# Performance work log

Hardware: AMD Instinct MI355X
Metric: run time of the kernel (lower is better)

The kernel has to match this reference:

```python
import jax, jax.numpy as jnp
import numpy as np

EPS = 1e-5  # BatchNorm1d default eps


def _bn(x):
    # BatchNorm1d(affine=False) in training mode: batch stats, biased variance
    m = x.mean(axis=0)
    v = ((x - m) ** 2).mean(axis=0)
    return (x - m) / jnp.sqrt(v + EPS)


def _gconv(x, A, W, b):
    # GraphConv with MeanAggregator: concat(x, A@x) @ W + b, ReLU
    agg = jnp.einsum('gnm,gmd->gnd', A, x)
    cat = jnp.concatenate([x, agg], axis=-1)
    return jax.nn.relu(jnp.einsum('gnd,df->gnf', cat, W) + b)


def setup_inputs() -> dict:
    key = jax.random.key(0)
    ks = jax.random.split(key, 16)
    B, C, H, Wd = 4, 32, 512, 512
    G, N, F = 512, 41, 576  # local graphs, 1+8+8*4 nodes, 3*4*(32+6)+120 feat
    d = {}
    d['inputs'] = jax.random.normal(ks[0], (B, C, H, Wd), jnp.float32)
    d['node_feats'] = jax.random.normal(ks[1], (G, N, F), jnp.float32)
    A = jax.random.uniform(ks[2], (G, N, N), jnp.float32)
    d['A'] = A / A.sum(-1, keepdims=True)  # row-normalized adjacency (mean agg)
    d['knn_inx'] = jax.random.randint(ks[3], (G, 8), 0, N)
    d['conv_w'] = jax.random.normal(ks[4], (6, C), jnp.float32) * 0.01
    d['conv_b'] = jnp.zeros((6,), jnp.float32)
    dims = [(2 * F, 512), (2 * 512, 256), (2 * 256, 128), (2 * 128, 64)]
    for i, (di, do) in enumerate(dims):
        d['W%d' % (i + 1)] = jax.random.normal(ks[5 + i], (di, do), jnp.float32) / np.float32(np.sqrt(di))
        d['b%d' % (i + 1)] = jnp.zeros((do,), jnp.float32)
    d['cls_w1'] = jax.random.normal(ks[10], (64, 32), jnp.float32) / 8.0
    d['cls_b1'] = jnp.zeros((32,), jnp.float32)
    d['prelu_a'] = jnp.full((32,), 0.25, jnp.float32)
    d['cls_w2'] = jax.random.normal(ks[11], (32, 2), jnp.float32) / np.float32(np.sqrt(32))
    d['cls_b2'] = jnp.zeros((2,), jnp.float32)
    return d


def reference(inputs, node_feats, A, knn_inx, conv_w, conv_b, W1, b1, W2, b2, W3, b3, W4, b4, cls_w1, cls_b1, prelu_a, cls_w2, cls_b2):
    # 1x1 conv: out_conv(inputs)
    pred_maps = jnp.einsum('bchw,oc->bohw', inputs, conv_w) + conv_b[None, :, None, None]
    # GCN over local graphs
    G, N, F = node_feats.shape
    x = _bn(node_feats.reshape(G * N, F)).reshape(G, N, F)
    x = _gconv(x, A, W1, b1)
    x = _gconv(x, A, W2, b2)
    x = _gconv(x, A, W3, b3)
    x = _gconv(x, A, W4, b4)
    # gather knn neighbor node features per graph -> edge features
    edge = jnp.take_along_axis(x, knn_inx[:, :, None], axis=1).reshape(-1, x.shape[-1])
    h = edge @ cls_w1 + cls_b1
    h = jnp.where(h >= 0, h, prelu_a * h)  # PReLU(32)
    gcn_pred = h @ cls_w2 + cls_b2  # [G*k, 2]
    return (pred_maps, gcn_pred)
```

## Files before the change

kernel.cpp:

```cpp
#include <hip/hip_runtime.h>
#include <hip/hip_bf16.h>


using f32x4 = __attribute__((ext_vector_type(4))) float;
using s16x8 = __attribute__((ext_vector_type(8))) short;

#define GN 20992
#define NFEAT 576
#define NGRAPH 512
#define NNODE 41
#define ASTR 44
#define NTMG 171

typedef __attribute__((address_space(1))) const unsigned int gas_u32;
typedef __attribute__((address_space(3))) unsigned int las_u32;

__device__ __forceinline__ void gl_lds16(const void* g, void* l) {
  __builtin_amdgcn_global_load_lds((gas_u32*)g, (las_u32*)l, 16, 0, 0);
}

__device__ __forceinline__ float dot41_f4(const float* __restrict__ Am,
                                          const float* __restrict__ pr) {
  float s0 = 0.f, s1 = 0.f, s2 = 0.f, s3 = 0.f;
#pragma unroll
  for (int q = 0; q < 10; ++q) {
    float4 a4 = *(const float4*)(Am + q * 4);
    s0 += a4.x * pr[q * 4];
    s1 += a4.y * pr[q * 4 + 1];
    s2 += a4.z * pr[q * 4 + 2];
    s3 += a4.w * pr[q * 4 + 3];
  }
  return ((s0 + s1) + (s2 + s3)) + Am[40] * pr[40];
}

__global__ __launch_bounds__(576) void front_kernel(
    const float* __restrict__ nf, float* __restrict__ partial,
    __hip_bfloat16* __restrict__ x0) {
  int c = threadIdx.x;
  int u = blockIdx.x;
  int r0 = u * 82;
  const float* src = nf + (size_t)r0 * NFEAT + c;
  __hip_bfloat16* dst = x0 + (size_t)r0 * NFEAT + c;
  float s = 0.f, s2 = 0.f;
#pragma unroll 4
  for (int r = 0; r < 82; ++r) {
    float v = src[(size_t)r * NFEAT];
    s += v; s2 += v * v;
    dst[(size_t)r * NFEAT] = __float2bfloat16(v);
  }
  partial[(size_t)u * 1152 + c] = s;
  partial[(size_t)u * 1152 + NFEAT + c] = s2;
}

__global__ __launch_bounds__(256) void reduce_kernel(
    const float* __restrict__ partial, float* __restrict__ statsbuf) {
  int t = blockIdx.x * 256 + threadIdx.x;
  if (t >= NFEAT) return;
  float s = 0.f, s2 = 0.f;
#pragma unroll 8
  for (int u = 0; u < 256; ++u) {
    s += partial[(size_t)u * 1152 + t];
    s2 += partial[(size_t)u * 1152 + NFEAT + t];
  }
  float m = s * (1.f / GN);
  float v = s2 * (1.f / GN) - m * m;
  float inv = rsqrtf(v + 1e-5f);
  statsbuf[t] = inv;
  statsbuf[NFEAT + t] = m * inv;
}

__global__ __launch_bounds__(256) void wt1_kernel(
    const float* __restrict__ W1, const float* __restrict__ b1,
    const float* __restrict__ statsbuf, __hip_bfloat16* __restrict__ B1,
    float* __restrict__ gbias,
    const float* __restrict__ W2, const float* __restrict__ W3,
    const float* __restrict__ W4,
    __hip_bfloat16* __restrict__ B2, __hip_bfloat16* __restrict__ B3,
    __hip_bfloat16* __restrict__ B4) {
  int u = blockIdx.x;
  int tid = threadIdx.x;
  if (u < 576) {
    __shared__ float T[32 * 33];
    int jt = u / 18, kt = u - jt * 18;
    int j0 = jt * 32, k0 = kt * 32;
    int h = (j0 >= 512) ? 1 : 0;
    const float* Wh = W1 + (size_t)(h * 576) * 512 + (j0 - h * 512);
    int r = tid >> 5, cc = tid & 31;
#pragma unroll
    for (int i = 0; i < 4; ++i)
      T[(r + i * 8) * 33 + cc] = Wh[(size_t)(k0 + r + i * 8) * 512 + cc];
    __syncthreads();
    float invv = statsbuf[k0 + cc];
#pragma unroll
    for (int i = 0; i < 4; ++i) {
      int rowh = (j0 - h * 512) + r + i * 8;
      int jp = (rowh >> 6) * 128 + h * 64 + (rowh & 63);
      B1[(size_t)jp * 576 + k0 + cc] =
          __float2bfloat16(T[cc * 33 + (r + i * 8)] * invv);
    }
  } else if (u < 580) {
    int j = (u - 576) * 256 + tid;
    int col = (j < 512) ? j : j - 512;
    const float* base = W1 + (size_t)((j < 512) ? 0 : 576) * 512 + col;
    float s = 0.f;
#pragma unroll 4
    for (int f = 0; f < NFEAT; ++f) s += statsbuf[NFEAT + f] * base[(size_t)f * 512];
    gbias[j] = ((j < 512) ? b1[j] : 0.f) - s;
  } else {
    __shared__ float T[32 * 33];
    int t = u - 580;
    const float* W; __hip_bfloat16* B; int K, N;
    if (t < 256)      { W = W2; B = B2; K = 512; N = 256; }
    else if (t < 320) { W = W3; B = B3; K = 256; N = 128; t -= 256; }
    else              { W = W4; B = B4; K = 128; N = 64;  t -= 320; }
    int tilesN = N >> 5;
    int perhalf = (K >> 5) * tilesN;
    int h = t / perhalf; t -= h * perhalf;
    int tk = t / tilesN, tn = t - tk * tilesN;
    int r = tid >> 5, cc = tid & 31;
    const float* Wh = W + (size_t)h * K * N;
#pragma unroll
    for (int i = 0; i < 4; ++i)
      T[(r + i * 8) * 33 + cc] = Wh[(size_t)(tk * 32 + r + i * 8) * N + tn * 32 + cc];
    __syncthreads();
#pragma unroll
    for (int i = 0; i < 4; ++i) {
      int row = tn * 32 + r + i * 8;
      int jp = (row >> 6) * 128 + h * 64 + (row & 63);
      B[(size_t)jp * K + tk * 32 + cc] =
          __float2bfloat16(T[cc * 33 + r + i * 8]);
    }
  }
}

__global__ __launch_bounds__(256) void gemmagg_kernel(
    const __hip_bfloat16* __restrict__ Xptr, const __hip_bfloat16* __restrict__ Bt,
    const float* __restrict__ biasL, const float* __restrict__ biasR,
    __hip_bfloat16* __restrict__ Yptr, int Nout, int K, int NTN,
    const float* __restrict__ Aadj,
    const float* __restrict__ cinputs, const float* __restrict__ conv_w,
    const float* __restrict__ conv_b, float* __restrict__ cout) {
  __shared__ __align__(16) char smem[53136];
  short* AshD = (short*)smem;
  short* BshD = (short*)(smem + 16384);
  __hip_bfloat16* Psh = (__hip_bfloat16*)smem;
  float* Aash = (float*)(smem + 31488);

  int tid = threadIdx.x;
  int bid = blockIdx.x;
  int gemmBlocks = NTMG * NTN;

  if (bid >= gemmBlocks) {
    int p = (bid - gemmBlocks) * 256 + tid;
    int img = p >> 16, q = p & 65535;
    const float4* ip = (const float4*)cinputs + (size_t)img * 32 * 65536 + q;
    float4 acc[6];
#pragma unroll
    for (int o = 0; o < 6; ++o) { float b0 = conv_b[o]; acc[o] = make_float4(b0, b0, b0, b0); }
#pragma unroll 4
    for (int c = 0; c < 32; ++c) {
      float4 x = ip[(size_t)c * 65536];
#pragma unroll
      for (int o = 0; o < 6; ++o) {
        float wv = conv_w[o * 32 + c];
        acc[o].x += x.x * wv; acc[o].y += x.y * wv;
        acc[o].z += x.z * wv; acc[o].w += x.w * wv;
      }
    }
    float4* op = (float4*)cout + (size_t)img * 6 * 65536 + q;
#pragma unroll
    for (int o = 0; o < 6; ++o) op[(size_t)o * 65536] = acc[o];
    return;
  }

  int sg = bid / (NTN * 8);
  int rem = bid - sg * (NTN * 8);
  int Wm = NTMG - sg * 8; if (Wm > 8) Wm = 8;
  int mt = sg * 8 + rem % Wm;
  int nt = rem / Wm;
  int row0 = mt * 123;
  int g0 = mt * 3;
  int gcnt = NGRAPH - g0; if (gcnt > 3) gcnt = 3;

  int wave = tid >> 6, lane = tid & 63;
  int wm = wave >> 1, wn = wave & 1;
  int lr = lane & 15, kb = lane >> 4;

  f32x4 acc[4][4];
#pragma unroll
  for (int m = 0; m < 4; ++m)
#pragma unroll
    for (int n = 0; n < 4; ++n) acc[m][n] = (f32x4){0.f, 0.f, 0.f, 0.f};

  const short* Ag = (const short*)Xptr;
  const short* Bg = (const short*)Bt + (size_t)nt * 128 * K;

  int c0 = tid, c1 = tid + 256;
  int ar0 = c0 >> 2, ak0 = (((c0 & 3) ^ ((ar0 >> 1) & 3))) * 8;
  int ar1 = c1 >> 2, ak1 = (((c1 & 3) ^ ((ar1 >> 1) & 3))) * 8;
  int grow0 = row0 + ar0; if (grow0 > GN - 1) grow0 = GN - 1;
  int grow1 = row0 + ar1; if (grow1 > GN - 1) grow1 = GN - 1;

  int aoff[4], boff[4];
#pragma unroll
  for (int m = 0; m < 4; ++m) {
    int r = wm * 64 + m * 16 + lr;
    aoff[m] = r * 32 + ((((r >> 1) & 3) ^ kb) * 8);
  }
#pragma unroll
  for (int n = 0; n < 4; ++n) {
    int r = wn * 64 + n * 16 + lr;
    boff[n] = r * 32 + ((((r >> 1) & 3) ^ kb) * 8);
  }

  gl_lds16(Ag + (size_t)grow0 * K + ak0, &AshD[c0 * 8]);
  gl_lds16(Ag + (size_t)grow1 * K + ak1, &AshD[c1 * 8]);
  gl_lds16(Bg + (size_t)ar0 * K + ak0, &BshD[c0 * 8]);
  gl_lds16(Bg + (size_t)ar1 * K + ak1, &BshD[c1 * 8]);
  __syncthreads();

  int nkt = K >> 5;
  int cur = 0;
  for (int kt = 0; kt < nkt; ++kt) {
    if (kt + 1 < nkt) {
      int k1 = (kt + 1) * 32;
      int nxt = (cur ^ 1) * 4096;
      gl_lds16(Ag + (size_t)grow0 * K + k1 + ak0, &AshD[nxt + c0 * 8]);
      gl_lds16(Ag + (size_t)grow1 * K + k1 + ak1, &AshD[nxt + c1 * 8]);
      gl_lds16(Bg + (size_t)ar0 * K + k1 + ak0, &BshD[nxt + c0 * 8]);
      gl_lds16(Bg + (size_t)ar1 * K + k1 + ak1, &BshD[nxt + c1 * 8]);
    }
    int cb = cur * 4096;
    s16x8 af[4], bfr[4];
#pragma unroll
    for (int m = 0; m < 4; ++m) af[m] = *(const s16x8*)&AshD[cb + aoff[m]];
#pragma unroll
    for (int n = 0; n < 4; ++n) bfr[n] = *(const s16x8*)&BshD[cb + boff[n]];
#pragma unroll
    for (int m = 0; m < 4; ++m)
#pragma unroll
      for (int n = 0; n < 4; ++n)
        acc[m][n] = __builtin_amdgcn_mfma_f32_16x16x32_bf16(af[m], bfr[n], acc[m][n], 0, 0, 0);
    __syncthreads();
    cur ^= 1;
  }

  int rbase = (lane >> 4) * 4;
#pragma unroll
  for (int m = 0; m < 4; ++m) {
    int lrow = wm * 64 + m * 16 + rbase;
#pragma unroll
    for (int n = 0; n < 4; ++n) {
      int w = wn * 64 + n * 16 + lr;
      float bv = (w < 64) ? biasL[nt * 64 + w]
                          : (biasR ? biasR[nt * 64 + (w - 64)] : 0.f);
#pragma unroll
      for (int r = 0; r < 4; ++r)
        Psh[(size_t)(lrow + r) * 128 + w] = __float2bfloat16(acc[m][n][r] + bv);
    }
  }
  __syncthreads();

  {
    int tot = gcnt * (NNODE * NNODE);
    const float* Asrc = Aadj + (size_t)g0 * (NNODE * NNODE);
    for (int i = tid; i < tot; i += 256) {
      int row = i / NNODE, m = i - row * NNODE;
      Aash[row * ASTR + m] = Asrc[i];
    }
  }
  __syncthreads();

  int c = tid & 63, grp = tid >> 6;
  for (int g = 0; g < gcnt; ++g) {
    float pr[NNODE];
#pragma unroll
    for (int m = 0; m < NNODE; ++m)
      pr[m] = __bfloat162float(Psh[(size_t)(g * NNODE + m) * 128 + 64 + c]);
#pragma unroll 1
    for (int n = grp; n < NNODE; n += 4) {
      float aa = __bfloat162float(Psh[(size_t)(g * NNODE + n) * 128 + c])
               + dot41_f4(Aash + (g * NNODE + n) * ASTR, pr);
      aa = aa > 0.f ? aa : 0.f;
      Yptr[(size_t)(row0 + g * NNODE + n) * Nout + nt * 64 + c] = __float2bfloat16(aa);
    }
  }
}

__global__ __launch_bounds__(256) void gemm4cls_kernel(
    const __hip_bfloat16* __restrict__ X, const __hip_bfloat16* __restrict__ B4t,
    const float* __restrict__ b4, const float* __restrict__ Aadj,
    const int* __restrict__ knn, const float* __restrict__ w1,
    const float* __restrict__ cb1, const float* __restrict__ pa,
    const float* __restrict__ w2, const float* __restrict__ cb2,
    float* __restrict__ out) {
  __shared__ __align__(16) char smem[49152 + 21648 + 31488 + 8192 + 520];
  short* AshD = (short*)smem;
  short* Bsh  = (short*)(smem + 16384);
  __hip_bfloat16* Psh = (__hip_bfloat16*)smem;
  float* Aash = (float*)(smem + 49152);
  float* Ysh  = (float*)(smem + 49152 + 21648);
  float* Wsh  = (float*)(smem + 49152 + 21648 + 31488);
  float* cb   = (float*)(smem + 49152 + 21648 + 31488 + 8192);

  int tid = threadIdx.x;
  int blk = blockIdx.x;
  int g0 = blk * 3;
  int gcnt = NGRAPH - g0; if (gcnt > 3) gcnt = 3;
  int row0 = blk * 123;

  {
    int tot = gcnt * (NNODE * NNODE);
    const float* Asrc = Aadj + (size_t)g0 * (NNODE * NNODE);
    for (int i = tid; i < tot; i += 256) {
      int row = i / NNODE, m = i - row * NNODE;
      Aash[row * ASTR + m] = Asrc[i];
    }
  }
  for (int i = tid; i < 2048; i += 256) Wsh[i] = w1[i];
  if (tid < 32) { cb[tid] = cb1[tid]; cb[32 + tid] = pa[tid]; }
  if (tid < 64) cb[64 + tid] = w2[tid];
  if (tid < 2) cb[128 + tid] = cb2[tid];

#pragma unroll
  for (int i = 0; i < 8; ++i) {
    int c = tid + i * 256;
    int kt = c >> 9, w = c & 511;
    int r = w >> 2, kc = ((w & 3) ^ ((r >> 1) & 3)) * 8;
    gl_lds16((const short*)B4t + (size_t)r * 128 + kt * 32 + kc, &Bsh[c * 8]);
  }
  const short* Ag = (const short*)X;
  int c0 = tid, c1 = tid + 256;
  int ar0 = c0 >> 2, ak0 = (((c0 & 3) ^ ((ar0 >> 1) & 3))) * 8;
  int ar1 = c1 >> 2, ak1 = (((c1 & 3) ^ ((ar1 >> 1) & 3))) * 8;
  int grow0 = row0 + ar0; if (grow0 > GN - 1) grow0 = GN - 1;
  int grow1 = row0 + ar1; if (grow1 > GN - 1) grow1 = GN - 1;
  gl_lds16(Ag + (size_t)grow0 * 128 + ak0, &AshD[c0 * 8]);
  gl_lds16(Ag + (size_t)grow1 * 128 + ak1, &AshD[c1 * 8]);
  __syncthreads();

  int wave = tid >> 6, lane = tid & 63;
  int wm = wave >> 1, wn = wave & 1;
  int lr = lane & 15, kb = lane >> 4;
  int aoff[4], boff[4];
#pragma unroll
  for (int m = 0; m < 4; ++m) {
    int r = wm * 64 + m * 16 + lr;
    aoff[m] = r * 32 + ((((r >> 1) & 3) ^ kb) * 8);
  }
#pragma unroll
  for (int n = 0; n < 4; ++n) {
    int r = wn * 64 + n * 16 + lr;
    boff[n] = r * 32 + ((((r >> 1) & 3) ^ kb) * 8);
  }
  f32x4 acc[4][4];
#pragma unroll
  for (int m = 0; m < 4; ++m)
#pragma unroll
    for (int n = 0; n < 4; ++n) acc[m][n] = (f32x4){0.f, 0.f, 0.f, 0.f};

  int cur = 0;
  for (int kt = 0; kt < 4; ++kt) {
    if (kt < 3) {
      int k1 = (kt + 1) * 32;
      int nxt = (cur ^ 1) * 4096;
      gl_lds16(Ag + (size_t)grow0 * 128 + k1 + ak0, &AshD[nxt + c0 * 8]);
      gl_lds16(Ag + (size_t)grow1 * 128 + k1 + ak1, &AshD[nxt + c1 * 8]);
    }
    int cbse = cur * 4096;
    s16x8 af[4], bfr[4];
#pragma unroll
    for (int m = 0; m < 4; ++m) af[m] = *(const s16x8*)&AshD[cbse + aoff[m]];
#pragma unroll
    for (int n = 0; n < 4; ++n) bfr[n] = *(const s16x8*)&Bsh[kt * 4096 + boff[n]];
#pragma unroll
    for (int m = 0; m < 4; ++m)
#pragma unroll
      for (int n = 0; n < 4; ++n)
        acc[m][n] = __builtin_amdgcn_mfma_f32_16x16x32_bf16(af[m], bfr[n], acc[m][n], 0, 0, 0);
    __syncthreads();
    cur ^= 1;
  }
  int rbase = (lane >> 4) * 4;
#pragma unroll
  for (int m = 0; m < 4; ++m) {
    int lrow = wm * 64 + m * 16 + rbase;
#pragma unroll
    for (int n = 0; n < 4; ++n) {
      int col = wn * 64 + n * 16 + lr;
      float bv = (col < 64) ? b4[col] : 0.f;
#pragma unroll
      for (int r = 0; r < 4; ++r)
        Psh[(size_t)(lrow + r) * 128 + col] = __float2bfloat16(acc[m][n][r] + bv);
    }
  }
  __syncthreads();

  int c = tid & 63, grp = tid >> 6;
  for (int g = 0; g < gcnt; ++g) {
    float pr[NNODE];
#pragma unroll
    for (int m = 0; m < NNODE; ++m)
      pr[m] = __bfloat162float(Psh[(size_t)(g * NNODE + m) * 128 + 64 + c]);
#pragma unroll 1
    for (int n = grp; n < NNODE; n += 4) {
      float aa = __bfloat162float(Psh[(size_t)(g * NNODE + n) * 128 + c])
               + dot41_f4(Aash + (g * NNODE + n) * ASTR, pr);
      Ysh[(g * NNODE + n) * 64 + c] = aa > 0.f ? aa : 0.f;
    }
  }
  __syncthreads();

  int j = tid & 31, slot = tid >> 5;
  for (int el = slot; el < 8 * gcnt; el += 8) {
    int e = g0 * 8 + el;
    int node = knn[e];
    int gl = el >> 3;
    const float* fp = &Ysh[(gl * NNODE + node) * 64];
    float a2 = cb[j];
#pragma unroll
    for (int d = 0; d < 64; ++d) a2 += fp[d] * Wsh[d * 32 + j];
    float h = a2 >= 0.f ? a2 : cb[32 + j] * a2;
#pragma unroll
    for (int o = 0; o < 2; ++o) {
      float v = h * cb[64 + j * 2 + o];
      v += __shfl_xor(v, 16, 32); v += __shfl_xor(v, 8, 32);
      v += __shfl_xor(v, 4, 32);  v += __shfl_xor(v, 2, 32);
      v += __shfl_xor(v, 1, 32);
      if (j == 0) out[(size_t)e * 2 + o] = v;
    }
  }
}

extern "C" void kernel_launch(void* const* d_in, const int* in_sizes, int n_in,
                              void* d_out, int out_size, void* d_ws, size_t ws_size,
                              hipStream_t stream) {
  const float* inputs     = (const float*)d_in[0];
  const float* node_feats = (const float*)d_in[1];
  const float* Aadj       = (const float*)d_in[2];
  const int*   knn        = (const int*)d_in[3];
  const float* conv_w     = (const float*)d_in[4];
  const float* conv_b     = (const float*)d_in[5];
  const float* W1 = (const float*)d_in[6];  const float* b1 = (const float*)d_in[7];
  const float* W2 = (const float*)d_in[8];  const float* b2 = (const float*)d_in[9];
  const float* W3 = (const float*)d_in[10]; const float* b3 = (const float*)d_in[11];
  const float* W4 = (const float*)d_in[12]; const float* b4 = (const float*)d_in[13];
  const float* cls_w1 = (const float*)d_in[14]; const float* cls_b1 = (const float*)d_in[15];
  const float* prelu_a = (const float*)d_in[16];
  const float* cls_w2 = (const float*)d_in[17]; const float* cls_b2 = (const float*)d_in[18];
  float* out = (float*)d_out;

  char* ws = (char*)d_ws;
  char* R1 = ws;
  char* R2 = ws + 24200192;
  char* wp = ws + 24200192 + 42991616;
  __hip_bfloat16* B1t = (__hip_bfloat16*)wp;  wp += 1179648;
  __hip_bfloat16* B2t = (__hip_bfloat16*)wp;  wp += 524288;
  __hip_bfloat16* B3t = (__hip_bfloat16*)wp;  wp += 131072;
  __hip_bfloat16* B4t = (__hip_bfloat16*)wp;  wp += 32768;
  float* partial  = (float*)wp;               wp += 256 * 1152 * 4;
  float* statsbuf = (float*)wp;               wp += 1152 * 4;
  float* gbias    = (float*)wp;               wp += 1024 * 4;

  __hip_bfloat16* x0 = (__hip_bfloat16*)R1;

  front_kernel<<<256, 576, 0, stream>>>(node_feats, partial, x0);
  reduce_kernel<<<3, 256, 0, stream>>>(partial, statsbuf);
  wt1_kernel<<<932, 256, 0, stream>>>(W1, b1, statsbuf, B1t, gbias,
                                      W2, W3, W4, B2t, B3t, B4t);

  gemmagg_kernel<<<NTMG * 8 + 1024, 256, 0, stream>>>(
      x0, B1t, gbias, gbias + 512, (__hip_bfloat16*)R2, 512, 576, 8, Aadj,
      inputs, conv_w, conv_b, out);
  gemmagg_kernel<<<NTMG * 4, 256, 0, stream>>>(
      (__hip_bfloat16*)R2, B2t, b2, nullptr, (__hip_bfloat16*)R1, 256, 512, 4,
      Aadj, nullptr, nullptr, nullptr, nullptr);
  gemmagg_kernel<<<NTMG * 2, 256, 0, stream>>>(
      (__hip_bfloat16*)R1, B3t, b3, nullptr, (__hip_bfloat16*)R2, 128, 256, 2,
      Aadj, nullptr, nullptr, nullptr, nullptr);
  gemm4cls_kernel<<<171, 256, 0, stream>>>(
      (__hip_bfloat16*)R2, B4t, b4, Aadj, knn, cls_w1, cls_b1, prelu_a,
      cls_w2, cls_b2, out + 6291456);
}
```

Measured before the change: 239.2 us.

## Interleave conv blocks with GEMM blocks and shrink adjacency LDS to one graph

The fused first-layer kernel now interleaves the 1x1-conv blocks with the GEMM+aggregation blocks (odd block ids do conv) instead of appending them at the end, so memory-bound conv work overlaps the compute-bound GEMM across the grid. The adjacency tile in shared memory now holds one graph at a time and is reloaded per graph, which cuts LDS from about 53KB to 40KB per block for higher occupancy. One barrier before the first adjacency load is removed, since that region no longer overlaps Psh. Costs are extra barriers and reloads per graph inside the aggregation loop.

```diff
diff --git a/kernel.cpp b/kernel.cpp
--- a/kernel.cpp
+++ b/kernel.cpp
@@ -136,41 +136,48 @@
 __global__ __launch_bounds__(256) void gemmagg_kernel(
     const __hip_bfloat16* __restrict__ Xptr, const __hip_bfloat16* __restrict__ Bt,
     const float* __restrict__ biasL, const float* __restrict__ biasR,
-    __hip_bfloat16* __restrict__ Yptr, int Nout, int K, int NTN,
+    __hip_bfloat16* __restrict__ Yptr, int Nout, int K, int NTN, int convBlocks,
     const float* __restrict__ Aadj,
     const float* __restrict__ cinputs, const float* __restrict__ conv_w,
     const float* __restrict__ conv_b, float* __restrict__ cout) {
-  __shared__ __align__(16) char smem[53136];
+  __shared__ __align__(16) char smem[39984];
   short* AshD = (short*)smem;
   short* BshD = (short*)(smem + 16384);
   __hip_bfloat16* Psh = (__hip_bfloat16*)smem;
-  float* Aash = (float*)(smem + 31488);
+  float* Aash = (float*)(smem + 32768);
 
   int tid = threadIdx.x;
   int bid = blockIdx.x;
-  int gemmBlocks = NTMG * NTN;
-
-  if (bid >= gemmBlocks) {
-    int p = (bid - gemmBlocks) * 256 + tid;
-    int img = p >> 16, q = p & 65535;
-    const float4* ip = (const float4*)cinputs + (size_t)img * 32 * 65536 + q;
-    float4 acc[6];
-#pragma unroll
-    for (int o = 0; o < 6; ++o) { float b0 = conv_b[o]; acc[o] = make_float4(b0, b0, b0, b0); }
+
+  if (convBlocks > 0) {
+    int twoC = convBlocks * 2;
+    if (bid < twoC) {
+      if (bid & 1) {
+        int p = (bid >> 1) * 256 + tid;
+        int img = p >> 16, q = p & 65535;
+        const float4* ip = (const float4*)cinputs + (size_t)img * 32 * 65536 + q;
+        float4 acc[6];
+#pragma unroll
+        for (int o = 0; o < 6; ++o) { float b0 = conv_b[o]; acc[o] = make_float4(b0, b0, b0, b0); }
 #pragma unroll 4
-    for (int c = 0; c < 32; ++c) {
-      float4 x = ip[(size_t)c * 65536];
-#pragma unroll
-      for (int o = 0; o < 6; ++o) {
-        float wv = conv_w[o * 32 + c];
-        acc[o].x += x.x * wv; acc[o].y += x.y * wv;
-        acc[o].z += x.z * wv; acc[o].w += x.w * wv;
+        for (int c = 0; c < 32; ++c) {
+          float4 x = ip[(size_t)c * 65536];
+#pragma unroll
+          for (int o = 0; o < 6; ++o) {
+            float wv = conv_w[o * 32 + c];
+            acc[o].x += x.x * wv; acc[o].y += x.y * wv;
+            acc[o].z += x.z * wv; acc[o].w += x.w * wv;
+          }
+        }
+        float4* op = (float4*)cout + (size_t)img * 6 * 65536 + q;
+#pragma unroll
+        for (int o = 0; o < 6; ++o) op[(size_t)o * 65536] = acc[o];
+        return;
       }
-    }
-    float4* op = (float4*)cout + (size_t)img * 6 * 65536 + q;
-#pragma unroll
-    for (int o = 0; o < 6; ++o) op[(size_t)o * 65536] = acc[o];
-    return;
+      bid >>= 1;
+    } else {
+      bid -= convBlocks;
+    }
   }
 
   int sg = bid / (NTN * 8);
@@ -259,12 +266,9 @@
         Psh[(size_t)(lrow + r) * 128 + w] = __float2bfloat16(acc[m][n][r] + bv);
     }
   }
-  __syncthreads();
-
   {
-    int tot = gcnt * (NNODE * NNODE);
     const float* Asrc = Aadj + (size_t)g0 * (NNODE * NNODE);
-    for (int i = tid; i < tot; i += 256) {
+    for (int i = tid; i < NNODE * NNODE; i += 256) {
       int row = i / NNODE, m = i - row * NNODE;
       Aash[row * ASTR + m] = Asrc[i];
     }
@@ -280,9 +284,18 @@
 #pragma unroll 1
     for (int n = grp; n < NNODE; n += 4) {
       float aa = __bfloat162float(Psh[(size_t)(g * NNODE + n) * 128 + c])
-               + dot41_f4(Aash + (g * NNODE + n) * ASTR, pr);
+               + dot41_f4(Aash + n * ASTR, pr);
       aa = aa > 0.f ? aa : 0.f;
       Yptr[(size_t)(row0 + g * NNODE + n) * Nout + nt * 64 + c] = __float2bfloat16(aa);
+    }
+    if (g + 1 < gcnt) {
+      __syncthreads();
+      const float* Asrc = Aadj + (size_t)(g0 + g + 1) * (NNODE * NNODE);
+      for (int i = tid; i < NNODE * NNODE; i += 256) {
+        int row = i / NNODE, m = i - row * NNODE;
+        Aash[row * ASTR + m] = Asrc[i];
+      }
+      __syncthreads();
     }
   }
 }
@@ -470,14 +483,14 @@
                                       W2, W3, W4, B2t, B3t, B4t);
 
   gemmagg_kernel<<<NTMG * 8 + 1024, 256, 0, stream>>>(
-      x0, B1t, gbias, gbias + 512, (__hip_bfloat16*)R2, 512, 576, 8, Aadj,
-      inputs, conv_w, conv_b, out);
+      x0, B1t, gbias, gbias + 512, (__hip_bfloat16*)R2, 512, 576, 8, 1024,
+      Aadj, inputs, conv_w, conv_b, out);
   gemmagg_kernel<<<NTMG * 4, 256, 0, stream>>>(
       (__hip_bfloat16*)R2, B2t, b2, nullptr, (__hip_bfloat16*)R1, 256, 512, 4,
-      Aadj, nullptr, nullptr, nullptr, nullptr);
+      0, Aadj, nullptr, nullptr, nullptr, nullptr);
   gemmagg_kernel<<<NTMG * 2, 256, 0, stream>>>(
       (__hip_bfloat16*)R1, B3t, b3, nullptr, (__hip_bfloat16*)R2, 128, 256, 2,
-      Aadj, nullptr, nullptr, nullptr, nullptr);
+      0, Aadj, nullptr, nullptr, nullptr, nullptr);
   gemm4cls_kernel<<<171, 256, 0, stream>>>(
       (__hip_bfloat16*)R2, B4t, b4, Aadj, knn, cls_w1, cls_b1, prelu_a,
       cls_w2, cls_b2, out + 6291456);
```

Result: slower. 286.6 us (+19.8%).
